# Kernel tuning notes

Hardware: AMD Instinct MI355X
Metric: run time of the kernel (lower is better)

The kernel has to match this reference:

```python
import jax, jax.numpy as jnp
import numpy as np

FEAT_DIM = 512
N_NODES = 65536


def setup_inputs() -> dict:
    key = jax.random.key(0)
    kq, kk, kv, ko = jax.random.split(key, 4)
    # scale inputs so exp(omega @ x) stays well within fp32 range
    Q = jax.random.normal(kq, (N_NODES, FEAT_DIM), dtype=jnp.float32) * 0.1
    K = jax.random.normal(kk, (N_NODES, FEAT_DIM), dtype=jnp.float32) * 0.1
    V = jax.random.normal(kv, (N_NODES, FEAT_DIM), dtype=jnp.float32)
    # omega = Gram-Schmidt (QR) orthogonalization of a Gaussian matrix, as in make_rand_feats
    G = jax.random.normal(ko, (FEAT_DIM, FEAT_DIM), dtype=jnp.float32)
    omega, _ = jnp.linalg.qr(G)
    return {"Q": Q, "K": K, "V": V, "omega": omega}


def _make_phi(x, omega):
    # omega_x[k, i] = sum_j omega[i, j] * x[k, j]  ->  x @ omega^T, shape [n, m]
    omega_x = x @ omega.T
    m = omega_x.shape[1]
    # h = exp(-||x||^2 / 2), shape [n, 1]
    h = jnp.exp(-0.5 * jnp.sum(x * x, axis=-1, keepdims=True))
    return (h / jnp.sqrt(jnp.float32(m))) * jnp.exp(omega_x)


def reference(Q, K, V, omega):
    Q_hat = _make_phi(Q, omega)  # [n, m]
    K_hat = _make_phi(K, omega)  # [n, m]
    # k_ones = K_hat^T @ 1  (column sums), shape [m]
    k_ones = jnp.sum(K_hat, axis=0)
    # d_diag = Q_hat @ k_ones, shape [n]; division replaces the n x n diag matmul
    d_diag = Q_hat @ k_ones
    kv = K_hat.T @ V            # [m, d_v]
    qkv = Q_hat @ kv            # [n, d_v]
    return qkv / d_diag[:, None]
```

## Files before the change

kernel.cpp:

```cpp
#include <hip/hip_runtime.h>
#include <hip/hip_bf16.h>


typedef __bf16 bf16x8 __attribute__((ext_vector_type(8)));
typedef float f32x4 __attribute__((ext_vector_type(4)));
typedef unsigned short ushort_t;
typedef ushort_t u16x8 __attribute__((ext_vector_type(8)));
typedef ushort_t u16x4 __attribute__((ext_vector_type(4)));

#define N_NODES 65536
#define FEAT 512

__device__ __forceinline__ ushort_t f2b(float f) {
  unsigned u = __builtin_bit_cast(unsigned, f);
  unsigned r = (u + 0x7fffu + ((u >> 16) & 1u)) >> 16;
  return (ushort_t)r;
}
__device__ __forceinline__ float b2f(ushort_t u) {
  return __builtin_bit_cast(float, ((unsigned)u) << 16);
}

__device__ __forceinline__ void load16(const ushort_t* g, ushort_t* l) {
  __builtin_amdgcn_global_load_lds((const __attribute__((address_space(1))) void*)g,
                                   (__attribute__((address_space(3))) void*)l, 16, 0, 0);
}

__device__ __forceinline__ void gemm_tile(const ushort_t* A, const ushort_t* B,
                                          long lda, long ldb, int ksteps,
                                          ushort_t* lA, ushort_t* lB, f32x4 acc[4][4]) {
  const int tid = threadIdx.x;
  const int lane = tid & 63;
  const int wid = tid >> 6;
  const int wr = wid >> 1, wc = wid & 1;
  const int lrow = lane & 15;
  const int lk8 = (lane >> 4) * 8;

  for (int kt = 0; kt < ksteps; ++kt) {
    const ushort_t* Ak = A + (size_t)kt * 64;
    const ushort_t* Bk = B + (size_t)kt * 64;
#pragma unroll
    for (int r = 0; r < 4; ++r) {
      int slot = tid + r * 256;
      int row = slot >> 3;
      int col = (slot & 7) * 8;
      load16(Ak + (size_t)row * lda + col, lA + slot * 8);
      load16(Bk + (size_t)row * ldb + col, lB + slot * 8);
    }
    __syncthreads();
#pragma unroll
    for (int ks = 0; ks < 2; ++ks) {
      bf16x8 af[4], bb[4];
#pragma unroll
      for (int mi = 0; mi < 4; ++mi)
        af[mi] = *(const bf16x8*)(lA + ((wr * 64 + mi * 16 + lrow) * 64 + ks * 32 + lk8));
#pragma unroll
      for (int ni = 0; ni < 4; ++ni)
        bb[ni] = *(const bf16x8*)(lB + ((wc * 64 + ni * 16 + lrow) * 64 + ks * 32 + lk8));
#pragma unroll
      for (int mi = 0; mi < 4; ++mi)
#pragma unroll
        for (int ni = 0; ni < 4; ++ni)
          acc[mi][ni] = __builtin_amdgcn_mfma_f32_16x16x32_bf16(af[mi], bb[ni], acc[mi][ni], 0, 0, 0);
    }
    __syncthreads();
  }
}

__global__ __launch_bounds__(256) void k_prep_x(const float* __restrict__ X,
                                                ushort_t* __restrict__ Xb,
                                                float* __restrict__ cX) {
  int wid = threadIdx.x >> 6, lane = threadIdx.x & 63;
  size_t row = (size_t)blockIdx.x * 4 + wid;
  const float4* xr = (const float4*)(X + row * FEAT);
  float4 a = xr[lane], b = xr[lane + 64];
  float s = a.x * a.x + a.y * a.y + a.z * a.z + a.w * a.w
          + b.x * b.x + b.y * b.y + b.z * b.z + b.w * b.w;
#pragma unroll
  for (int off = 32; off; off >>= 1) s += __shfl_xor(s, off, 64);
  u16x4 pa = {f2b(a.x), f2b(a.y), f2b(a.z), f2b(a.w)};
  u16x4 pb = {f2b(b.x), f2b(b.y), f2b(b.z), f2b(b.w)};
  u16x4* xo = (u16x4*)(Xb + row * FEAT);
  xo[lane] = pa;
  xo[lane + 64] = pb;
  if (lane == 0) cX[row] = -0.5f * s - 3.11916231f;
}

__global__ __launch_bounds__(256) void k_prep_omega(const float* __restrict__ om,
                                                    ushort_t* __restrict__ Ob) {
  int i = blockIdx.x * 256 + threadIdx.x;
  float4 v = ((const float4*)om)[i];
  u16x4 o = {f2b(v.x), f2b(v.y), f2b(v.z), f2b(v.w)};
  ((u16x4*)Ob)[i] = o;
}

__global__ __launch_bounds__(256) void k_vt(const float* __restrict__ V,
                                            ushort_t* __restrict__ VT) {
  __shared__ ushort_t t[64][72];
  int r0 = blockIdx.x * 64;
  int c0 = blockIdx.y * 64;
#pragma unroll
  for (int it = 0; it < 4; ++it) {
    int slot = threadIdx.x + it * 256;
    int r = slot >> 4;
    int c4 = slot & 15;
    float4 v = *(const float4*)(V + (size_t)(r0 + r) * FEAT + c0 + c4 * 4);
    u16x4 p = {f2b(v.x), f2b(v.y), f2b(v.z), f2b(v.w)};
    *(u16x4*)&t[r][c4 * 4] = p;
  }
  __syncthreads();
#pragma unroll
  for (int it = 0; it < 2; ++it) {
    int slot = threadIdx.x + it * 256;
    int dr = slot >> 3;
    int n8 = slot & 7;
    u16x8 o;
#pragma unroll
    for (int j = 0; j < 8; ++j) o[j] = t[n8 * 8 + j][dr];
    *(u16x8*)(VT + (size_t)(c0 + dr) * N_NODES + r0 + n8 * 8) = o;
  }
}

__global__ __launch_bounds__(256) void k_phi(const ushort_t* __restrict__ Xb,
                                             const ushort_t* __restrict__ Ob,
                                             const float* __restrict__ cX,
                                             ushort_t* __restrict__ Out, int transposed) {
  __shared__ ushort_t lA[128 * 64], lB[128 * 64];
  f32x4 acc[4][4];
#pragma unroll
  for (int i = 0; i < 4; ++i)
#pragma unroll
    for (int j = 0; j < 4; ++j) acc[i][j] = (f32x4){0.f, 0.f, 0.f, 0.f};
  const int m0 = blockIdx.y * 128, n0 = blockIdx.x * 128;
  gemm_tile(Xb + (size_t)m0 * FEAT, Ob + (size_t)n0 * FEAT, FEAT, FEAT, 8, lA, lB, acc);

  const int lane = threadIdx.x & 63, wid = threadIdx.x >> 6;
  const int wr = wid >> 1, wc = wid & 1;
  const int cbase = n0 + wc * 64 + (lane & 15);
  const int rbase = m0 + wr * 64 + ((lane >> 4) << 2);
#pragma unroll
  for (int mi = 0; mi < 4; ++mi) {
    int r0 = rbase + mi * 16;
    float cv[4];
#pragma unroll
    for (int j = 0; j < 4; ++j) cv[j] = cX[r0 + j];
#pragma unroll
    for (int ni = 0; ni < 4; ++ni) {
      int col = cbase + ni * 16;
      if (transposed) {
        u16x4 pk;
#pragma unroll
        for (int j = 0; j < 4; ++j) pk[j] = f2b(__expf(acc[mi][ni][j] + cv[j]));
        *(u16x4*)(Out + (size_t)col * N_NODES + r0) = pk;
      } else {
#pragma unroll
        for (int j = 0; j < 4; ++j)
          Out[(size_t)(r0 + j) * FEAT + col] = f2b(__expf(acc[mi][ni][j] + cv[j]));
      }
    }
  }
}

__global__ __launch_bounds__(256) void k_rowsum(const ushort_t* __restrict__ KT,
                                                float* __restrict__ k1) {
  const ushort_t* row = KT + (size_t)blockIdx.x * N_NODES;
  float s = 0.f;
  for (int i = threadIdx.x; i < N_NODES / 8; i += 256) {
    u16x8 v = ((const u16x8*)row)[i];
#pragma unroll
    for (int j = 0; j < 8; ++j) s += b2f(v[j]);
  }
#pragma unroll
  for (int off = 32; off; off >>= 1) s += __shfl_xor(s, off, 64);
  __shared__ float wsum[4];
  int lane = threadIdx.x & 63, wid = threadIdx.x >> 6;
  if (lane == 0) wsum[wid] = s;
  __syncthreads();
  if (threadIdx.x == 0) k1[blockIdx.x] = wsum[0] + wsum[1] + wsum[2] + wsum[3];
}

__global__ __launch_bounds__(256) void k_kv(const ushort_t* __restrict__ KT,
                                            const ushort_t* __restrict__ VT,
                                            float* __restrict__ P) {
  __shared__ ushort_t lA[128 * 64], lB[128 * 64];
  f32x4 acc[4][4];
#pragma unroll
  for (int i = 0; i < 4; ++i)
#pragma unroll
    for (int j = 0; j < 4; ++j) acc[i][j] = (f32x4){0.f, 0.f, 0.f, 0.f};
  const int m0 = blockIdx.y * 128, n0 = blockIdx.x * 128, z = blockIdx.z;
  gemm_tile(KT + (size_t)m0 * N_NODES + z * 2048,
            VT + (size_t)n0 * N_NODES + z * 2048, N_NODES, N_NODES, 32, lA, lB, acc);
  float* Pz = P + (size_t)z * (FEAT * FEAT);
  const int lane = threadIdx.x & 63, wid = threadIdx.x >> 6;
  const int wr = wid >> 1, wc = wid & 1;
  const int cbase = n0 + wc * 64 + (lane & 15);
  const int rbase = m0 + wr * 64 + ((lane >> 4) << 2);
#pragma unroll
  for (int mi = 0; mi < 4; ++mi)
#pragma unroll
    for (int ni = 0; ni < 4; ++ni)
#pragma unroll
      for (int j = 0; j < 4; ++j)
        Pz[(size_t)(rbase + mi * 16 + j) * FEAT + cbase + ni * 16] = acc[mi][ni][j];
}

__global__ __launch_bounds__(256) void k_redkv(const float* __restrict__ P,
                                               ushort_t* __restrict__ kvT) {
  int t = blockIdx.x * 256 + threadIdx.x;
  int m = t >> 7;
  int d4 = t & 127;
  float4 s = {0.f, 0.f, 0.f, 0.f};
  for (int z = 0; z < 32; ++z) {
    float4 v = *(const float4*)(P + (size_t)z * (FEAT * FEAT) + (size_t)m * FEAT + d4 * 4);
    s.x += v.x; s.y += v.y; s.z += v.z; s.w += v.w;
  }
  kvT[(size_t)(d4 * 4 + 0) * FEAT + m] = f2b(s.x);
  kvT[(size_t)(d4 * 4 + 1) * FEAT + m] = f2b(s.y);
  kvT[(size_t)(d4 * 4 + 2) * FEAT + m] = f2b(s.z);
  kvT[(size_t)(d4 * 4 + 3) * FEAT + m] = f2b(s.w);
}

__global__ __launch_bounds__(256) void k_dd(const ushort_t* __restrict__ Qh,
                                            const float* __restrict__ k1,
                                            float* __restrict__ dd) {
  int rid = threadIdx.x >> 4, l16 = threadIdx.x & 15;
  int row = blockIdx.x * 16 + rid;
  const ushort_t* qr = Qh + (size_t)row * FEAT;
  float s = 0.f;
#pragma unroll
  for (int it = 0; it < 4; ++it) {
    int cb = it * 128 + l16 * 8;
    u16x8 q = *(const u16x8*)(qr + cb);
    float4 ka = *(const float4*)(k1 + cb);
    float4 kb = *(const float4*)(k1 + cb + 4);
    s += b2f(q[0]) * ka.x + b2f(q[1]) * ka.y + b2f(q[2]) * ka.z + b2f(q[3]) * ka.w
       + b2f(q[4]) * kb.x + b2f(q[5]) * kb.y + b2f(q[6]) * kb.z + b2f(q[7]) * kb.w;
  }
  s += __shfl_xor(s, 1, 64); s += __shfl_xor(s, 2, 64);
  s += __shfl_xor(s, 4, 64); s += __shfl_xor(s, 8, 64);
  if (l16 == 0) dd[row] = s;
}

__global__ __launch_bounds__(256) void k_final(const ushort_t* __restrict__ Qh,
                                               const ushort_t* __restrict__ kvT,
                                               const float* __restrict__ dd,
                                               float* __restrict__ out) {
  __shared__ ushort_t lA[128 * 64], lB[128 * 64];
  f32x4 acc[4][4];
#pragma unroll
  for (int i = 0; i < 4; ++i)
#pragma unroll
    for (int j = 0; j < 4; ++j) acc[i][j] = (f32x4){0.f, 0.f, 0.f, 0.f};
  const int m0 = blockIdx.y * 128, n0 = blockIdx.x * 128;
  gemm_tile(Qh + (size_t)m0 * FEAT, kvT + (size_t)n0 * FEAT, FEAT, FEAT, 8, lA, lB, acc);
  const int lane = threadIdx.x & 63, wid = threadIdx.x >> 6;
  const int wr = wid >> 1, wc = wid & 1;
  const int cbase = n0 + wc * 64 + (lane & 15);
  const int rbase = m0 + wr * 64 + ((lane >> 4) << 2);
#pragma unroll
  for (int mi = 0; mi < 4; ++mi) {
    int r0 = rbase + mi * 16;
    float inv[4];
#pragma unroll
    for (int j = 0; j < 4; ++j) inv[j] = 1.0f / dd[r0 + j];
#pragma unroll
    for (int ni = 0; ni < 4; ++ni) {
      int col = cbase + ni * 16;
#pragma unroll
      for (int j = 0; j < 4; ++j)
        out[(size_t)(r0 + j) * FEAT + col] = acc[mi][ni][j] * inv[j];
    }
  }
}

extern "C" void kernel_launch(void* const* d_in, const int* in_sizes, int n_in,
                              void* d_out, int out_size, void* d_ws, size_t ws_size,
                              hipStream_t stream) {
  const float* Q = (const float*)d_in[0];
  const float* K = (const float*)d_in[1];
  const float* V = (const float*)d_in[2];
  const float* omega = (const float*)d_in[3];
  float* out = (float*)d_out;

  char* ws = (char*)d_ws;
  ushort_t* B1  = (ushort_t*)(ws);
  ushort_t* B2  = (ushort_t*)(ws + 67108864);
  ushort_t* Ob  = (ushort_t*)(ws + 134217728);
  ushort_t* kvT = (ushort_t*)(ws + 134742016);
  float*    k1  = (float*)(ws + 135266304);
  float*    cX  = (float*)(ws + 135268352);
  float*    dd  = (float*)(ws + 135530496);
  float*    P   = (float*)d_out;

  k_prep_x<<<N_NODES / 4, 256, 0, stream>>>(K, B1, cX);
  k_prep_omega<<<256, 256, 0, stream>>>(omega, Ob);
  k_phi<<<dim3(4, 512), 256, 0, stream>>>(B1, Ob, cX, B2, 1);
  k_rowsum<<<512, 256, 0, stream>>>(B2, k1);
  k_vt<<<dim3(N_NODES / 64, 8), 256, 0, stream>>>(V, B1);
  k_kv<<<dim3(4, 4, 32), 256, 0, stream>>>(B2, B1, P);
  k_prep_x<<<N_NODES / 4, 256, 0, stream>>>(Q, B1, cX);
  k_phi<<<dim3(4, 512), 256, 0, stream>>>(B1, Ob, cX, B2, 0);
  k_redkv<<<256, 256, 0, stream>>>(P, kvT);
  k_dd<<<N_NODES / 16, 256, 0, stream>>>(B2, k1, dd);
  k_final<<<dim3(4, 512), 256, 0, stream>>>(B2, kvT, dd, out);
}
```

Baseline: 685.6 us.

## Fuse fp32-to-bf16 prep, norm, and column/row reductions into phi GEMM kernels

The separate prep, rowsum and d_diag kernels are removed. The phi GEMM now loads fp32 X directly, converts it to bf16 into LDS and accumulates squared norms on the fly. Its epilogue atomically accumulates K_hat column sums, or Q_hat·k1 row dots for d_diag, which avoids writing and re-reading bf16 intermediates. The cost is that each of the 4 column blocks re-reads and re-converts the fp32 X tile, the A load no longer goes straight to LDS, and atomics make the reductions nondeterministic.

```diff
diff --git a/kernel.cpp b/kernel.cpp
--- a/kernel.cpp
+++ b/kernel.cpp
@@ -23,6 +23,11 @@
 __device__ __forceinline__ void load16(const ushort_t* g, ushort_t* l) {
   __builtin_amdgcn_global_load_lds((const __attribute__((address_space(1))) void*)g,
                                    (__attribute__((address_space(3))) void*)l, 16, 0, 0);
+}
+
+__global__ __launch_bounds__(256) void k_zero(float* __restrict__ p, int n) {
+  int i = blockIdx.x * 256 + threadIdx.x;
+  if (i < n) p[i] = 0.f;
 }
 
 __device__ __forceinline__ void gemm_tile(const ushort_t* A, const ushort_t* B,
@@ -66,25 +71,6 @@
   }
 }
 
-__global__ __launch_bounds__(256) void k_prep_x(const float* __restrict__ X,
-                                                ushort_t* __restrict__ Xb,
-                                                float* __restrict__ cX) {
-  int wid = threadIdx.x >> 6, lane = threadIdx.x & 63;
-  size_t row = (size_t)blockIdx.x * 4 + wid;
-  const float4* xr = (const float4*)(X + row * FEAT);
-  float4 a = xr[lane], b = xr[lane + 64];
-  float s = a.x * a.x + a.y * a.y + a.z * a.z + a.w * a.w
-          + b.x * b.x + b.y * b.y + b.z * b.z + b.w * b.w;
-#pragma unroll
-  for (int off = 32; off; off >>= 1) s += __shfl_xor(s, off, 64);
-  u16x4 pa = {f2b(a.x), f2b(a.y), f2b(a.z), f2b(a.w)};
-  u16x4 pb = {f2b(b.x), f2b(b.y), f2b(b.z), f2b(b.w)};
-  u16x4* xo = (u16x4*)(Xb + row * FEAT);
-  xo[lane] = pa;
-  xo[lane + 64] = pb;
-  if (lane == 0) cX[row] = -0.5f * s - 3.11916231f;
-}
-
 __global__ __launch_bounds__(256) void k_prep_omega(const float* __restrict__ om,
                                                     ushort_t* __restrict__ Ob) {
   int i = blockIdx.x * 256 + threadIdx.x;
@@ -120,62 +106,137 @@
   }
 }
 
-__global__ __launch_bounds__(256) void k_phi(const ushort_t* __restrict__ Xb,
-                                             const ushort_t* __restrict__ Ob,
-                                             const float* __restrict__ cX,
-                                             ushort_t* __restrict__ Out, int transposed) {
+template <int TRANSK>
+__global__ __launch_bounds__(256) void k_phi_fused(const float* __restrict__ X,
+                                                   const ushort_t* __restrict__ Ob,
+                                                   const float* __restrict__ k1,
+                                                   float* __restrict__ k1w,
+                                                   float* __restrict__ dd,
+                                                   ushort_t* __restrict__ Out) {
   __shared__ ushort_t lA[128 * 64], lB[128 * 64];
+  __shared__ float cvbuf[128];
   f32x4 acc[4][4];
 #pragma unroll
   for (int i = 0; i < 4; ++i)
 #pragma unroll
     for (int j = 0; j < 4; ++j) acc[i][j] = (f32x4){0.f, 0.f, 0.f, 0.f};
+
+  const int tid = threadIdx.x;
+  const int lane = tid & 63;
+  const int wid = tid >> 6;
+  const int wr = wid >> 1, wc = wid & 1;
+  const int lrow = lane & 15;
+  const int lk8 = (lane >> 4) * 8;
   const int m0 = blockIdx.y * 128, n0 = blockIdx.x * 128;
-  gemm_tile(Xb + (size_t)m0 * FEAT, Ob + (size_t)n0 * FEAT, FEAT, FEAT, 8, lA, lB, acc);
-
-  const int lane = threadIdx.x & 63, wid = threadIdx.x >> 6;
-  const int wr = wid >> 1, wc = wid & 1;
-  const int cbase = n0 + wc * 64 + (lane & 15);
-  const int rbase = m0 + wr * 64 + ((lane >> 4) << 2);
+  const float* Ax = X + (size_t)m0 * FEAT;
+  const ushort_t* Bo = Ob + (size_t)n0 * FEAT;
+  const int arow = tid >> 3;
+  const int acol = (tid & 7) * 8;
+  float nacc[4] = {0.f, 0.f, 0.f, 0.f};
+
+  for (int kt = 0; kt < 8; ++kt) {
+#pragma unroll
+    for (int r = 0; r < 4; ++r) {
+      int slot = tid + r * 256;
+      int row = slot >> 3;
+      int col = (slot & 7) * 8;
+      load16(Bo + (size_t)row * FEAT + kt * 64 + col, lB + slot * 8);
+    }
+#pragma unroll
+    for (int r = 0; r < 4; ++r) {
+      int row = arow + r * 32;
+      const float* src = Ax + (size_t)row * FEAT + kt * 64 + acol;
+      float4 a0 = *(const float4*)src;
+      float4 a1 = *(const float4*)(src + 4);
+      nacc[r] += a0.x * a0.x + a0.y * a0.y + a0.z * a0.z + a0.w * a0.w
+               + a1.x * a1.x + a1.y * a1.y + a1.z * a1.z + a1.w * a1.w;
+      u16x8 p = {f2b(a0.x), f2b(a0.y), f2b(a0.z), f2b(a0.w),
+                 f2b(a1.x), f2b(a1.y), f2b(a1.z), f2b(a1.w)};
+      *(u16x8*)(lA + (size_t)(tid + r * 256) * 8) = p;
+    }
+    __syncthreads();
+#pragma unroll
+    for (int ks = 0; ks < 2; ++ks) {
+      bf16x8 af[4], bb[4];
+#pragma unroll
+      for (int mi = 0; mi < 4; ++mi)
+        af[mi] = *(const bf16x8*)(lA + ((wr * 64 + mi * 16 + lrow) * 64 + ks * 32 + lk8));
+#pragma unroll
+      for (int ni = 0; ni < 4; ++ni)
+        bb[ni] = *(const bf16x8*)(lB + ((wc * 64 + ni * 16 + lrow) * 64 + ks * 32 + lk8));
+#pragma unroll
+      for (int mi = 0; mi < 4; ++mi)
+#pragma unroll
+        for (int ni = 0; ni < 4; ++ni)
+          acc[mi][ni] = __builtin_amdgcn_mfma_f32_16x16x32_bf16(af[mi], bb[ni], acc[mi][ni], 0, 0, 0);
+    }
+    __syncthreads();
+  }
+
+#pragma unroll
+  for (int r = 0; r < 4; ++r) {
+    float s = nacc[r];
+    s += __shfl_xor(s, 1, 64);
+    s += __shfl_xor(s, 2, 64);
+    s += __shfl_xor(s, 4, 64);
+    if ((lane & 7) == 0) cvbuf[arow + r * 32] = -0.5f * s - 3.11916231f;
+  }
+  __syncthreads();
+
+  const int cbase = n0 + wc * 64 + lrow;
+  const int lrbase = wr * 64 + ((lane >> 4) << 2);
+  float colp[4] = {0.f, 0.f, 0.f, 0.f};
+  float k1v[4];
+  if (!TRANSK) {
+#pragma unroll
+    for (int ni = 0; ni < 4; ++ni) k1v[ni] = k1[cbase + ni * 16];
+  }
 #pragma unroll
   for (int mi = 0; mi < 4; ++mi) {
-    int r0 = rbase + mi * 16;
+    int lr0 = lrbase + mi * 16;
     float cv[4];
 #pragma unroll
-    for (int j = 0; j < 4; ++j) cv[j] = cX[r0 + j];
+    for (int j = 0; j < 4; ++j) cv[j] = cvbuf[lr0 + j];
+    if (TRANSK) {
+#pragma unroll
+      for (int ni = 0; ni < 4; ++ni) {
+        int col = cbase + ni * 16;
+        u16x4 pk;
+#pragma unroll
+        for (int j = 0; j < 4; ++j) {
+          float e = __expf(acc[mi][ni][j] + cv[j]);
+          pk[j] = f2b(e);
+          colp[ni] += e;
+        }
+        *(u16x4*)(Out + (size_t)col * N_NODES + m0 + lr0) = pk;
+      }
+    } else {
+#pragma unroll
+      for (int j = 0; j < 4; ++j) {
+        float t = 0.f;
+#pragma unroll
+        for (int ni = 0; ni < 4; ++ni) {
+          float e = __expf(acc[mi][ni][j] + cv[j]);
+          Out[(size_t)(m0 + lr0 + j) * FEAT + cbase + ni * 16] = f2b(e);
+          t += e * k1v[ni];
+        }
+        t += __shfl_xor(t, 1, 64);
+        t += __shfl_xor(t, 2, 64);
+        t += __shfl_xor(t, 4, 64);
+        t += __shfl_xor(t, 8, 64);
+        if (lrow == 0) atomicAdd(&dd[m0 + lr0 + j], t);
+      }
+    }
+  }
+  if (TRANSK) {
 #pragma unroll
     for (int ni = 0; ni < 4; ++ni) {
-      int col = cbase + ni * 16;
-      if (transposed) {
-        u16x4 pk;
-#pragma unroll
-        for (int j = 0; j < 4; ++j) pk[j] = f2b(__expf(acc[mi][ni][j] + cv[j]));
-        *(u16x4*)(Out + (size_t)col * N_NODES + r0) = pk;
-      } else {
-#pragma unroll
-        for (int j = 0; j < 4; ++j)
-          Out[(size_t)(r0 + j) * FEAT + col] = f2b(__expf(acc[mi][ni][j] + cv[j]));
-      }
-    }
-  }
-}
-
-__global__ __launch_bounds__(256) void k_rowsum(const ushort_t* __restrict__ KT,
-                                                float* __restrict__ k1) {
-  const ushort_t* row = KT + (size_t)blockIdx.x * N_NODES;
-  float s = 0.f;
-  for (int i = threadIdx.x; i < N_NODES / 8; i += 256) {
-    u16x8 v = ((const u16x8*)row)[i];
-#pragma unroll
-    for (int j = 0; j < 8; ++j) s += b2f(v[j]);
-  }
-#pragma unroll
-  for (int off = 32; off; off >>= 1) s += __shfl_xor(s, off, 64);
-  __shared__ float wsum[4];
-  int lane = threadIdx.x & 63, wid = threadIdx.x >> 6;
-  if (lane == 0) wsum[wid] = s;
-  __syncthreads();
-  if (threadIdx.x == 0) k1[blockIdx.x] = wsum[0] + wsum[1] + wsum[2] + wsum[3];
+      float t = colp[ni];
+      t += __shfl_xor(t, 16, 64);
+      t += __shfl_xor(t, 32, 64);
+      if (lane < 16) atomicAdd(&k1w[n0 + wc * 64 + lane + ni * 16], t);
+    }
+  }
 }
 
 __global__ __launch_bounds__(256) void k_kv(const ushort_t* __restrict__ KT,
@@ -220,27 +281,6 @@
   kvT[(size_t)(d4 * 4 + 3) * FEAT + m] = f2b(s.w);
 }
 
-__global__ __launch_bounds__(256) void k_dd(const ushort_t* __restrict__ Qh,
-                                            const float* __restrict__ k1,
-                                            float* __restrict__ dd) {
-  int rid = threadIdx.x >> 4, l16 = threadIdx.x & 15;
-  int row = blockIdx.x * 16 + rid;
-  const ushort_t* qr = Qh + (size_t)row * FEAT;
-  float s = 0.f;
-#pragma unroll
-  for (int it = 0; it < 4; ++it) {
-    int cb = it * 128 + l16 * 8;
-    u16x8 q = *(const u16x8*)(qr + cb);
-    float4 ka = *(const float4*)(k1 + cb);
-    float4 kb = *(const float4*)(k1 + cb + 4);
-    s += b2f(q[0]) * ka.x + b2f(q[1]) * ka.y + b2f(q[2]) * ka.z + b2f(q[3]) * ka.w
-       + b2f(q[4]) * kb.x + b2f(q[5]) * kb.y + b2f(q[6]) * kb.z + b2f(q[7]) * kb.w;
-  }
-  s += __shfl_xor(s, 1, 64); s += __shfl_xor(s, 2, 64);
-  s += __shfl_xor(s, 4, 64); s += __shfl_xor(s, 8, 64);
-  if (l16 == 0) dd[row] = s;
-}
-
 __global__ __launch_bounds__(256) void k_final(const ushort_t* __restrict__ Qh,
                                                const ushort_t* __restrict__ kvT,
                                                const float* __restrict__ dd,
@@ -288,19 +328,15 @@
   ushort_t* Ob  = (ushort_t*)(ws + 134217728);
   ushort_t* kvT = (ushort_t*)(ws + 134742016);
   float*    k1  = (float*)(ws + 135266304);
-  float*    cX  = (float*)(ws + 135268352);
-  float*    dd  = (float*)(ws + 135530496);
+  float*    dd  = (float*)(ws + 135268352);
   float*    P   = (float*)d_out;
 
-  k_prep_x<<<N_NODES / 4, 256, 0, stream>>>(K, B1, cX);
+  k_zero<<<(512 + 65536 + 255) / 256, 256, 0, stream>>>(k1, 512 + 65536);
   k_prep_omega<<<256, 256, 0, stream>>>(omega, Ob);
-  k_phi<<<dim3(4, 512), 256, 0, stream>>>(B1, Ob, cX, B2, 1);
-  k_rowsum<<<512, 256, 0, stream>>>(B2, k1);
+  k_phi_fused<1><<<dim3(4, 512), 256, 0, stream>>>(K, Ob, k1, k1, dd, B2);
   k_vt<<<dim3(N_NODES / 64, 8), 256, 0, stream>>>(V, B1);
   k_kv<<<dim3(4, 4, 32), 256, 0, stream>>>(B2, B1, P);
-  k_prep_x<<<N_NODES / 4, 256, 0, stream>>>(Q, B1, cX);
-  k_phi<<<dim3(4, 512), 256, 0, stream>>>(B1, Ob, cX, B2, 0);
+  k_phi_fused<0><<<dim3(4, 512), 256, 0, stream>>>(Q, Ob, k1, k1, dd, B2);
   k_redkv<<<256, 256, 0, stream>>>(P, kvT);
-  k_dd<<<N_NODES / 16, 256, 0, stream>>>(B2, k1, dd);
   k_final<<<dim3(4, 512), 256, 0, stream>>>(B2, kvT, dd, out);
 }
```

Result: no change. 689.0 us (+0.5%).
